# Optimization experiments

Hardware: AMD Instinct MI355X
Metric: run time of the kernel (lower is better)

## Reference

```python
import jax, jax.numpy as jnp
import numpy as np


def setup_inputs() -> dict:
    bs, L, d, h = 4, 1024, 768, 12
    ne, nm, K, P, F, R = 42, 8, 97, 128, 256, 256
    key = jax.random.key(0)
    ks = jax.random.split(key, 16)
    seq = jax.random.normal(ks[0], (bs, L, d), jnp.float32)
    att = jax.random.uniform(ks[1], (bs, h, L, L), jnp.float32)
    mention_pos = jax.random.randint(ks[2], (bs, ne, nm), 0, 1000)
    n_men = jax.random.randint(ks[3], (bs, ne), 1, nm + 1)
    men_mask = (jnp.arange(nm)[None, None, :] < n_men[..., None]).astype(jnp.float32)
    ht_pairs = jax.random.randint(ks[4], (bs, P, 2), 0, ne)
    s = 0.02
    Wattn = jax.random.normal(ks[5], (d, R)) * s
    battn = jnp.zeros((R,), jnp.float32)
    attn_net = jax.random.normal(ks[6], (K, R)) * s
    Wlin = jax.random.normal(ks[7], (d, 3)) * s
    blin = jnp.zeros((3,), jnp.float32)
    Wseg = jax.random.normal(ks[8], (3, 3, 3, F)) * s  # HWIO conv kernel (SegNet stand-in)
    bseg = jnp.zeros((F,), jnp.float32)
    Whead = jax.random.normal(ks[9], (d + F, d)) * s
    bhead = jnp.zeros((d,), jnp.float32)
    Wtail = jax.random.normal(ks[10], (d + F, d)) * s
    btail = jnp.zeros((d,), jnp.float32)
    lim = (1.0 / (2 * d)) ** 0.5
    bilinear = jax.random.uniform(ks[11], (K, d, d), minval=-lim, maxval=lim)
    bilinear_bias = jax.random.uniform(ks[12], (K,), minval=-lim, maxval=lim)
    return dict(sequence_output=seq, attention=att, men_mask=men_mask,
                mention_pos=mention_pos, ht_pairs=ht_pairs,
                Wattn=Wattn, battn=battn, attn_net=attn_net, Wlin=Wlin, blin=blin,
                Wseg=Wseg, bseg=bseg, Whead=Whead, bhead=bhead, Wtail=Wtail,
                btail=btail, bilinear=bilinear, bilinear_bias=bilinear_bias)


def _forward(sequence_output, attention, men_mask, mention_pos, ht_pairs,
             Wattn, battn, attn_net, Wlin, blin, Wseg, bseg,
             Whead, bhead, Wtail, btail, bilinear, bilinear_bias):
    bs, L, d = sequence_output.shape
    h = attention.shape[1]
    ne, nm = mention_pos.shape[1], mention_pos.shape[2]
    K = attn_net.shape[0]
    OFFSET = 1  # BERT [CLS] offset
    pos = jnp.clip(mention_pos + OFFSET, 0, L - 1)           # [bs,ne,nm]
    b_idx = jnp.arange(bs)[:, None, None]
    # ragged mention gather from sequence_output, zero-padded like the torch loops
    emb = sequence_output[b_idx, pos] * men_mask[..., None]  # [bs,ne,nm,d]
    # per-mention attention rows; attention -> [bs,L,h,L] so we gather on token dim
    A = jnp.transpose(attention, (0, 2, 1, 3))
    m_att = A[b_idx, pos] * men_mask[..., None, None]        # [bs,ne,nm,h,L]
    cnt = jnp.maximum(men_mask.sum(-1), 1.0)                 # mentions per entity
    entity_as = m_att.sum(2) / cnt[..., None, None]          # [bs,ne,h,L] mean over mentions
    # label-wise masked attention pooling over mentions
    neg = (1.0 - men_mask)[..., None] * -1e6                 # [bs,ne,nm,1]
    scores = jnp.tanh(emb @ Wattn + battn) @ attn_net.T + neg  # [bs,ne,nm,K]
    w = jax.nn.softmax(scores, axis=-2)                      # softmax over mentions
    entity_es = jnp.einsum('benk,bend->bekd', w, emb)        # [bs,ne,K,d]
    # context-based channel map (pairwise attention overlap, mean over heads)
    ht = jnp.einsum('bihl,bjhl->bijl', entity_as, entity_as) / h  # [bs,ne,ne,L]
    ht = ht / (ht.sum(-1, keepdims=True) + 1e-5)
    fmap = jnp.einsum('bijl,bld->bijd', ht, sequence_output)      # [bs,ne,ne,d]
    x = fmap @ Wlin + blin                                        # [bs,ne,ne,3]
    seg = jax.lax.conv_general_dilated(x, Wseg, (1, 1), 'SAME',
                                       dimension_numbers=('NHWC', 'HWIO', 'NHWC'))
    attn_map = jax.nn.relu(seg + bseg)                            # [bs,ne,ne,F]
    # pairwise gather (get_hts)
    hi, ti = ht_pairs[..., 0], ht_pairs[..., 1]
    bI = jnp.arange(bs)[:, None]
    F = attn_map.shape[-1]
    htss = attn_map[bI, hi, ti].reshape(-1, F)               # [N,F]
    hss = entity_es[bI, hi].reshape(-1, K, d)                # [N,K,d]
    tss = entity_es[bI, ti].reshape(-1, K, d)
    N = hss.shape[0]
    htr = jnp.broadcast_to(htss[:, None, :], (N, K, F))
    hs = jnp.tanh(jnp.concatenate([hss, htr], -1) @ Whead + bhead)
    ts = jnp.tanh(jnp.concatenate([tss, htr], -1) @ Wtail + btail)
    logits = jnp.einsum('nkd,kdp,nkp->nk', hs, bilinear, ts) + bilinear_bias
    return logits


def reference(sequence_output, attention, men_mask, mention_pos, ht_pairs,
              Wattn, battn, attn_net, Wlin, blin, Wseg, bseg,
              Whead, bhead, Wtail, btail, bilinear, bilinear_bias):
    return _forward(sequence_output, attention, men_mask, mention_pos, ht_pairs,
                    Wattn, battn, attn_net, Wlin, blin, Wseg, bseg,
                    Whead, bhead, Wtail, btail, bilinear, bilinear_bias)
```

## Files before the change

### kernel.cpp

```cpp
#include <hip/hip_runtime.h>
#include <hip/hip_bf16.h>

#define BS 4
#define LL 1024
#define DD 768
#define HH 12
#define NE 42
#define NM 8
#define KK 97
#define PPAIR 128
#define FF 256
#define RR 256
#define NPAIR (BS*PPAIR)
#define MROWS (BS*NE*KK)
#define MT 510
#define NT32 16
#define GRID_BG (8*13*16)

typedef __attribute__((ext_vector_type(8))) short short8;
typedef __attribute__((ext_vector_type(16))) float float16;

__device__ __forceinline__ float fast_tanh(float x){
  x = fminf(fmaxf(x, -15.f), 15.f);
  float e = __expf(2.f*x);
  return 1.f - 2.f/(e + 1.f);
}
__device__ __forceinline__ unsigned short f2bf(float f){
  unsigned int u = __float_as_uint(f);
  unsigned int r = (u + 0x7FFF + ((u>>16)&1)) >> 16;
  return (unsigned short)r;
}
__device__ __forceinline__ float bf2f(unsigned short u){
  return __uint_as_float(((unsigned int)u)<<16);
}

__global__ void k_emb(const float* __restrict__ seq, const int* __restrict__ mpos,
                      const float* __restrict__ mask, float* __restrict__ emb){
  int idx = blockIdx.x;
  int t = threadIdx.x;
  int b = idx / (NE*NM);
  float mk = mask[idx];
  int pos = mpos[idx] + 1;
  pos = min(max(pos, 0), LL-1);
  const float* src = seq + ((size_t)b*LL + pos)*DD;
  float* dst = emb + (size_t)idx*DD;
  for (int dd = t; dd < DD; dd += 256) dst[dd] = mk * src[dd];
}

__global__ void k_entity_as(const float* __restrict__ att, const int* __restrict__ mpos,
                            const float* __restrict__ mask, float* __restrict__ eas){
  int idx = blockIdx.x;
  int hh = idx % HH; int be = idx / HH;
  int b = be / NE;
  int t = threadIdx.x;
  float cnt = 0.f;
  for (int m=0;m<NM;m++) cnt += mask[be*NM+m];
  float inv = 1.f / fmaxf(cnt, 1.f);
  float acc[4] = {0.f,0.f,0.f,0.f};
  for (int m=0;m<NM;m++){
    float mk = mask[be*NM+m];
    if (mk != 0.f){
      int pos = min(max(mpos[be*NM+m]+1,0), LL-1);
      const float* row = att + (((size_t)b*HH + hh)*LL + pos)*LL;
      acc[0] += mk*row[t]; acc[1] += mk*row[t+256];
      acc[2] += mk*row[t+512]; acc[3] += mk*row[t+768];
    }
  }
  float* dst = eas + (size_t)idx*LL;
  dst[t]=acc[0]*inv; dst[t+256]=acc[1]*inv; dst[t+512]=acc[2]*inv; dst[t+768]=acc[3]*inv;
}

__global__ void k_score1(const float* __restrict__ emb, const float* __restrict__ Wattn,
                         const float* __restrict__ battn, float* __restrict__ tbuf){
  int idx = blockIdx.x; int t = threadIdx.x;
  __shared__ float es[DD];
  es[t]       = emb[(size_t)idx*DD + t];
  es[t+256]   = emb[(size_t)idx*DD + t + 256];
  es[t+512]   = emb[(size_t)idx*DD + t + 512];
  __syncthreads();
  float acc = battn[t];
  for (int dd=0; dd<DD; dd++) acc += es[dd]*Wattn[dd*RR + t];
  tbuf[(size_t)idx*RR + t] = fast_tanh(acc);
}

__global__ void k_scores(const float* __restrict__ tbuf, const float* __restrict__ an,
                         const float* __restrict__ mask, float* __restrict__ w){
  int be = blockIdx.x; int t = threadIdx.x;
  __shared__ float ts_[NM*RR];
  __shared__ float an_s[64*98];
  for (int i=t; i<NM*RR; i+=128) ts_[i] = tbuf[(size_t)be*NM*RR + i];
  float acc[NM];
  #pragma unroll
  for (int m=0;m<NM;m++) acc[m] = 0.f;
  for (int rc=0; rc<RR; rc+=64){
    __syncthreads();
    for (int i=t; i<KK*64; i+=128){
      int kq = i >> 6, r = i & 63;
      an_s[r*98 + kq] = an[kq*RR + rc + r];
    }
    __syncthreads();
    if (t < KK){
      for (int m=0;m<NM;m++){
        float a = 0.f;
        for (int r=0;r<64;r++) a += ts_[m*RR + rc + r]*an_s[r*98 + t];
        acc[m] += a;
      }
    }
  }
  if (t < KK){
    float s[NM];
    #pragma unroll
    for (int m=0;m<NM;m++){
      float mk = mask[be*NM+m];
      s[m] = acc[m] + (1.f - mk)*(-1e6f);
    }
    float mx = s[0];
    #pragma unroll
    for (int m=1;m<NM;m++) mx = fmaxf(mx, s[m]);
    float sum = 0.f; float e[NM];
    #pragma unroll
    for (int m=0;m<NM;m++){ e[m] = __expf(s[m]-mx); sum += e[m]; }
    float invs = 1.f/sum;
    #pragma unroll
    for (int m=0;m<NM;m++) w[((size_t)be*NM+m)*KK + t] = e[m]*invs;
  }
}

__global__ void k_entity_es(const float* __restrict__ emb, const float* __restrict__ w,
                            unsigned short* __restrict__ esf){
  int be = blockIdx.x; int t = threadIdx.x;
  __shared__ float es[NM*DD];
  __shared__ float ws_[NM*KK];
  for (int i = t; i < NM*DD; i += 256) es[i] = emb[(size_t)be*NM*DD + i];
  for (int i = t; i < NM*KK; i += 256) ws_[i] = w[(size_t)be*NM*KK + i];
  __syncthreads();
  for (int idx = t; idx < KK*96; idx += 256){
    int k = idx % KK, d8 = idx / KK;
    int d0 = d8*8;
    float a[8] = {0,0,0,0,0,0,0,0};
    #pragma unroll
    for (int m=0;m<NM;m++){
      float wv = ws_[m*KK + k];
      #pragma unroll
      for (int j=0;j<8;j++) a[j] += wv*es[m*DD + d0 + j];
    }
    int row = be*KK + k;
    int mt = row >> 5, lr = row & 31, ds = d8 >> 1, qq = d8 & 1;
    short8 v;
    #pragma unroll
    for (int j=0;j<8;j++) v[j] = (short)f2bf(a[j]);
    *(short8*)(esf + ((((size_t)mt*48) + ds)*64 + lr + 32*qq)*8) = v;
  }
}

__global__ void k_seqlin(const float* __restrict__ seq, const float* __restrict__ Wlin,
                         float* __restrict__ sl){
  int bl = blockIdx.x; int t = threadIdx.x;
  const float* row = seq + (size_t)bl*DD;
  float a[3] = {0.f,0.f,0.f};
  for (int dd=t; dd<DD; dd+=256){
    float v = row[dd];
    a[0] += v*Wlin[dd*3+0]; a[1] += v*Wlin[dd*3+1]; a[2] += v*Wlin[dd*3+2];
  }
  __shared__ float red[256];
  float res[3];
  for (int c=0;c<3;c++){
    red[t] = a[c]; __syncthreads();
    for (int off=128; off>0; off>>=1){ if (t<off) red[t]+=red[t+off]; __syncthreads(); }
    res[c] = red[0]; __syncthreads();
  }
  if (t==0){ sl[bl*3+0]=res[0]; sl[bl*3+1]=res[1]; sl[bl*3+2]=res[2]; }
}

__global__ void k_ht_x(const float* __restrict__ eas, const float* __restrict__ sl,
                       const float* __restrict__ blin, float* __restrict__ x){
  int idx = blockIdx.x;
  int j = idx % NE; int i = (idx/NE)%NE; int b = idx/(NE*NE);
  int t = threadIdx.x;
  int w = t >> 6, lane = t & 63;
  const float* ai = eas + ((size_t)(b*NE+i))*HH*LL;
  const float* aj = eas + ((size_t)(b*NE+j))*HH*LL;
  float v[4];
  #pragma unroll
  for (int it=0; it<4; it++){
    int l = t + it*256;
    float acc=0.f;
    #pragma unroll
    for (int hh2=0; hh2<HH; hh2++) acc += ai[hh2*LL + l]*aj[hh2*LL + l];
    v[it] = acc * (1.f/HH);
  }
  __shared__ float wsum[4];
  __shared__ float xred[4][3];
  float s = v[0]+v[1]+v[2]+v[3];
  s += __shfl_xor(s, 1);  s += __shfl_xor(s, 2);  s += __shfl_xor(s, 4);
  s += __shfl_xor(s, 8);  s += __shfl_xor(s, 16); s += __shfl_xor(s, 32);
  if (lane == 0) wsum[w] = s;
  __syncthreads();
  float inv = 1.f/((wsum[0]+wsum[1]+wsum[2]+wsum[3]) + 1e-5f);
  float xa[3]={0.f,0.f,0.f};
  #pragma unroll
  for (int it=0; it<4; it++){
    int l = t + it*256;
    float wv = v[it]*inv;
    const float* s3 = sl + ((size_t)b*LL + l)*3;
    xa[0]+=wv*s3[0]; xa[1]+=wv*s3[1]; xa[2]+=wv*s3[2];
  }
  #pragma unroll
  for (int c=0;c<3;c++){
    float q = xa[c];
    q += __shfl_xor(q, 1);  q += __shfl_xor(q, 2);  q += __shfl_xor(q, 4);
    q += __shfl_xor(q, 8);  q += __shfl_xor(q, 16); q += __shfl_xor(q, 32);
    if (lane == 0) xred[w][c] = q;
  }
  __syncthreads();
  if (t < 3) x[(size_t)idx*3 + t] = xred[0][t]+xred[1][t]+xred[2][t]+xred[3][t] + blin[t];
}

__global__ void k_conv_pairs(const float* __restrict__ x, const int* __restrict__ pairs,
                             const float* __restrict__ Wseg, const float* __restrict__ bseg,
                             float* __restrict__ htss){
  int n = blockIdx.x; int t = threadIdx.x;
  int b = n / PPAIR;
  int hi = pairs[n*2+0], ti = pairs[n*2+1];
  __shared__ float xs[27];
  if (t < 27){
    int di = t/9, dj = (t/3)%3, ci = t%3;
    int ii = hi + di - 1, jj = ti + dj - 1;
    float v = 0.f;
    if (ii>=0 && ii<NE && jj>=0 && jj<NE) v = x[(((size_t)b*NE+ii)*NE+jj)*3 + ci];
    xs[t] = v;
  }
  __syncthreads();
  float acc = bseg[t];
  #pragma unroll
  for (int tap=0; tap<27; tap++) acc += xs[tap]*Wseg[tap*FF + t];
  htss[(size_t)n*FF + t] = fmaxf(acc, 0.f);
}

__global__ void k_pair_proj(const float* __restrict__ htss, const float* __restrict__ Wb,
                            const float* __restrict__ bias, float* __restrict__ outp){
  int n = blockIdx.x; int t = threadIdx.x;
  __shared__ float hs_s[FF];
  hs_s[t] = htss[(size_t)n*FF + t];
  __syncthreads();
  float a0 = bias[t], a1 = bias[t+256], a2 = bias[t+512];
  for (int r=0;r<FF;r++){
    float hv = hs_s[r];
    const float* wr = Wb + (size_t)r*DD;
    a0 += hv*wr[t]; a1 += hv*wr[t+256]; a2 += hv*wr[t+512];
  }
  float* dst = outp + (size_t)n*DD;
  dst[t]=a0; dst[t+256]=a1; dst[t+512]=a2;
}

__global__ void k_wshuffle(const float* __restrict__ src, unsigned short* __restrict__ dst){
  int bi = blockIdx.x;
  int mat = bi / 144; int r = bi % 144;
  int ds = r / 3, ntg = r % 3;
  int t = threadIdx.x;
  size_t mo = (size_t)mat*589824;
  __shared__ float ls[16][260];
  #pragma unroll
  for (int i=0;i<16;i++)
    ls[i][t] = src[mo + ((size_t)(ds*16+i))*768 + ntg*256 + t];
  __syncthreads();
  #pragma unroll
  for (int it=0; it<2; it++){
    int idx = it*256 + t;
    int pt_l = idx >> 6, lane = idx & 63;
    int nl = pt_l*32 + (lane & 31);
    int qq = lane >> 5;
    short8 v;
    #pragma unroll
    for (int j=0;j<8;j++) v[j] = (short)f2bf(ls[qq*8 + j][nl]);
    *(short8*)(dst + mo + (((size_t)ds*24 + ntg*8 + pt_l)*64 + lane)*8) = v;
  }
}

__global__ __launch_bounds__(256) void k_gemm_frag(const unsigned short* __restrict__ Af,
    const unsigned short* __restrict__ Bf, unsigned short* __restrict__ C){
  int mt = blockIdx.x / 6, ntg = blockIdx.x % 6;
  int t = threadIdx.x; int w = t >> 6; int lane = t & 63;
  int nt = ntg*4 + w;
  float16 acc = (float16)(0.0f);
  const unsigned short* ap = Af + (((size_t)mt*48)*64 + lane)*8;
  const unsigned short* bp = Bf + (((size_t)nt)*64 + lane)*8;
  #pragma unroll 4
  for (int ds=0; ds<48; ds++){
    short8 a = *(const short8*)(ap + (size_t)ds*512);
    short8 b = *(const short8*)(bp + (size_t)ds*24*512);
    acc = __builtin_amdgcn_mfma_f32_32x32x16_bf16(a, b, acc, 0, 0, 0);
  }
  int col = nt*32 + (lane & 31);
  int aq = lane >> 5;
  #pragma unroll
  for (int rI=0;rI<16;rI++){
    int row = mt*32 + (rI&3) + 8*(rI>>2) + 4*aq;
    C[(size_t)row*768 + col] = f2bf(acc[rI]);
  }
}

__global__ void k_hsts(const unsigned short* __restrict__ Ehb, const float* __restrict__ ph,
                       const int* __restrict__ pairs, unsigned short* __restrict__ hsF){
  int bi = blockIdx.x; int nt = bi / KK; int k = bi - nt*KK;
  int t = threadIdx.x;
  __shared__ int ehB[32];
  if (t < 32){
    int n = nt*32 + t; int b = n >> 7;
    ehB[t] = ((b*NE + pairs[n*2+0])*KK + k)*DD;
  }
  __syncthreads();
  unsigned short* dst = hsF + (((size_t)nt*KK + k)*48)*512;
  #pragma unroll 2
  for (int c=0; c<12; c++){
    int L = c*256 + t;
    int ds = L >> 6, lane = L & 63;
    int r = lane & 31, q = lane >> 5;
    int n = nt*32 + r;
    int d0 = ds*16 + q*8;
    short8 ev = *(const short8*)(Ehb + ehB[r] + d0);
    float4 p0 = *(const float4*)(ph + (size_t)n*DD + d0);
    float4 p1 = *(const float4*)(ph + (size_t)n*DD + d0 + 4);
    float pf[8] = {p0.x,p0.y,p0.z,p0.w,p1.x,p1.y,p1.z,p1.w};
    short8 v;
    #pragma unroll
    for (int j=0;j<8;j++) v[j] = (short)f2bf(fast_tanh(bf2f((unsigned short)ev[j]) + pf[j]));
    *(short8*)(dst + (size_t)ds*512 + lane*8) = v;
  }
}

__global__ void k_outinit(const float* __restrict__ bias, float* __restrict__ out){
  int i = blockIdx.x*256 + threadIdx.x;
  if (i < NPAIR*KK) out[i] = bias[i % KK];
}

__global__ __launch_bounds__(512,4) void k_bil_gemm(
    const unsigned short* __restrict__ hsF, const unsigned short* __restrict__ Etb,
    const float* __restrict__ pt_, const unsigned short* __restrict__ Bfrag,
    const int* __restrict__ pairs, float* __restrict__ out){
  int xcd = blockIdx.x & 7; int g = blockIdx.x >> 3;
  int ps = g & 3; int nt = (g >> 2) & 3; int kgrp = g >> 4;
  int k = kgrp*8 + xcd;
  if (k >= KK) return;
  int n0 = nt*128;
  int t = threadIdx.x; int w = t >> 6; int lane = t & 63;
  int wr = w >> 1, wc = w & 1;
  __shared__ int etB[128];
  __shared__ float redbuf[4][2][32];
  if (t < 128){
    int n = n0 + t; int b = n >> 7;
    etB[t] = ((b*NE + pairs[n*2+1])*KK + k)*DD;
  }
  __syncthreads();
  int aq = lane >> 5;
  int mt = nt*4 + wr;
  const unsigned short* ap = hsF + (((size_t)mt*KK + k)*48)*512 + lane*8;
  const unsigned short* bb = Bfrag + (size_t)k*589824 + (size_t)lane*8;
  int pb0 = ps*6 + wc;
  float16 acc0 = (float16)(0.f), acc1 = (float16)(0.f), acc2 = (float16)(0.f);
  #pragma unroll 4
  for (int ds=0; ds<48; ds++){
    short8 a = *(const short8*)(ap + (size_t)ds*512);
    const unsigned short* bds = bb + (size_t)ds*24*512;
    short8 b0 = *(const short8*)(bds + (size_t)(pb0+0)*512);
    short8 b1 = *(const short8*)(bds + (size_t)(pb0+2)*512);
    short8 b2 = *(const short8*)(bds + (size_t)(pb0+4)*512);
    acc0 = __builtin_amdgcn_mfma_f32_32x32x16_bf16(a, b0, acc0, 0, 0, 0);
    acc1 = __builtin_amdgcn_mfma_f32_32x32x16_bf16(a, b1, acc1, 0, 0, 0);
    acc2 = __builtin_amdgcn_mfma_f32_32x32x16_bf16(a, b2, acc2, 0, 0, 0);
  }
  #pragma unroll
  for (int rI=0; rI<16; rI++){
    int row = (rI&3) + 8*(rI>>2) + 4*aq;
    int nloc = wr*32 + row;
    int eb = etB[nloc];
    const float* ptp = pt_ + (size_t)(n0 + nloc)*DD;
    int colb = lane & 31;
    int c0 = (pb0+0)*32 + colb, c1 = (pb0+2)*32 + colb, c2 = (pb0+4)*32 + colb;
    float s = acc0[rI]*fast_tanh(bf2f(Etb[eb + c0]) + ptp[c0])
            + acc1[rI]*fast_tanh(bf2f(Etb[eb + c1]) + ptp[c1])
            + acc2[rI]*fast_tanh(bf2f(Etb[eb + c2]) + ptp[c2]);
    s += __shfl_xor(s, 1);  s += __shfl_xor(s, 2);
    s += __shfl_xor(s, 4);  s += __shfl_xor(s, 8);
    s += __shfl_xor(s, 16);
    if ((lane & 31) == 0) redbuf[wr][wc][row] = s;
  }
  __syncthreads();
  if (t < 128){
    atomicAdd(&out[(size_t)(n0 + t)*KK + k],
              redbuf[t>>5][0][t&31] + redbuf[t>>5][1][t&31]);
  }
}

extern "C" void kernel_launch(void* const* d_in, const int* in_sizes, int n_in,
                              void* d_out, int out_size, void* d_ws, size_t ws_size,
                              hipStream_t stream){
  const float* seq      = (const float*)d_in[0];
  const float* att      = (const float*)d_in[1];
  const float* mask     = (const float*)d_in[2];
  const int*   mpos     = (const int*)d_in[3];
  const int*   pairs    = (const int*)d_in[4];
  const float* Wattn    = (const float*)d_in[5];
  const float* battn    = (const float*)d_in[6];
  const float* attn_net = (const float*)d_in[7];
  const float* Wlin     = (const float*)d_in[8];
  const float* blin     = (const float*)d_in[9];
  const float* Wseg     = (const float*)d_in[10];
  const float* bseg     = (const float*)d_in[11];
  const float* Whead    = (const float*)d_in[12];
  const float* bhead    = (const float*)d_in[13];
  const float* Wtail    = (const float*)d_in[14];
  const float* btail    = (const float*)d_in[15];
  const float* bil      = (const float*)d_in[16];
  const float* bilb     = (const float*)d_in[17];
  float* out = (float*)d_out;

  char* ws = (char*)d_ws;
  size_t off = 0;
  auto allocB = [&](size_t nbytes)->char*{
    char* p = ws + off;
    off += (nbytes + 255) & ~(size_t)255;
    return p;
  };
  unsigned short* BF     = (unsigned short*)allocB((size_t)KK*589824*2);
  unsigned short* Ehb    = (unsigned short*)allocB((size_t)MT*32*768*2);
  unsigned short* Etb    = (unsigned short*)allocB((size_t)MT*32*768*2);
  unsigned short* WheadF = (unsigned short*)allocB((size_t)589824*2);
  unsigned short* WtailF = (unsigned short*)allocB((size_t)589824*2);
  float* phb  = (float*)allocB((size_t)NPAIR*DD*4);
  float* ptb  = (float*)allocB((size_t)NPAIR*DD*4);
  size_t hsF_bytes = (size_t)NT32*KK*48*512*2;
  char* uni = allocB(hsF_bytes);
  size_t uoff = 0;
  auto ualloc = [&](size_t nbytes)->char*{
    char* p = uni + uoff;
    uoff += (nbytes + 255) & ~(size_t)255;
    return p;
  };
  float* emb  = (float*)ualloc((size_t)BS*NE*NM*DD*4);
  float* tbuf = (float*)ualloc((size_t)BS*NE*NM*RR*4);
  float* wsm  = (float*)ualloc((size_t)BS*NE*NM*KK*4);
  float* eas  = (float*)ualloc((size_t)BS*NE*HH*LL*4);
  float* sl   = (float*)ualloc((size_t)BS*LL*3*4);
  float* xb   = (float*)ualloc((size_t)BS*NE*NE*3*4);
  float* htss = (float*)ualloc((size_t)NPAIR*FF*4);
  unsigned short* esf = (unsigned short*)ualloc((size_t)MT*48*64*8*2);
  unsigned short* hsF = (unsigned short*)uni;

  k_outinit<<<(NPAIR*KK+255)/256, 256, 0, stream>>>(bilb, out);
  k_emb<<<BS*NE*NM, 256, 0, stream>>>(seq, mpos, mask, emb);
  k_score1<<<BS*NE*NM, 256, 0, stream>>>(emb, Wattn, battn, tbuf);
  k_scores<<<BS*NE, 128, 0, stream>>>(tbuf, attn_net, mask, wsm);
  k_entity_as<<<BS*NE*HH, 256, 0, stream>>>(att, mpos, mask, eas);
  k_entity_es<<<BS*NE, 256, 0, stream>>>(emb, wsm, esf);
  k_seqlin<<<BS*LL, 256, 0, stream>>>(seq, Wlin, sl);
  k_ht_x<<<BS*NE*NE, 256, 0, stream>>>(eas, sl, blin, xb);
  k_conv_pairs<<<NPAIR, 256, 0, stream>>>(xb, pairs, Wseg, bseg, htss);
  k_pair_proj<<<NPAIR, 256, 0, stream>>>(htss, Whead + 768*768, bhead, phb);
  k_pair_proj<<<NPAIR, 256, 0, stream>>>(htss, Wtail + 768*768, btail, ptb);
  k_wshuffle<<<144, 256, 0, stream>>>(Whead, WheadF);
  k_wshuffle<<<144, 256, 0, stream>>>(Wtail, WtailF);
  k_wshuffle<<<KK*144, 256, 0, stream>>>(bil, BF);
  k_gemm_frag<<<MT*6, 256, 0, stream>>>(esf, WheadF, Ehb);
  k_gemm_frag<<<MT*6, 256, 0, stream>>>(esf, WtailF, Etb);
  k_hsts<<<NT32*KK, 256, 0, stream>>>(Ehb, phb, pairs, hsF);
  k_bil_gemm<<<GRID_BG, 512, 0, stream>>>(hsF, Etb, ptb, BF, pairs, out);
}
```

Before: 970.6 us.

## Stage bilinear GEMM tiles via LDS double buffering and fuse head/tail GEMMs

In the bilinear GEMM, operand fragments were loaded redundantly from global memory by each wave. They are now loaded once per block into LDS using async global_load_lds, with a two-stage double buffer and barriers. The head and tail projection GEMMs also merge into one kernel that reuses the A fragment for both weight sets. The aim is to cut global memory traffic and launches, at the cost of two barriers per k-step and hand-written waitcnt bookkeeping.

New measurement: 892.9 us. 1.09x faster.

```diff
diff --git a/kernel.cpp b/kernel.cpp
--- a/kernel.cpp
+++ b/kernel.cpp
@@ -32,6 +32,11 @@
 }
 __device__ __forceinline__ float bf2f(unsigned short u){
   return __uint_as_float(((unsigned int)u)<<16);
+}
+__device__ __forceinline__ void stage16(const void* g, void* l){
+  __builtin_amdgcn_global_load_lds(
+      (const __attribute__((address_space(1))) void*)g,
+      (__attribute__((address_space(3))) void*)l, 16, 0, 0);
 }
 
 __global__ void k_emb(const float* __restrict__ seq, const int* __restrict__ mpos,
@@ -277,26 +282,31 @@
   }
 }
 
-__global__ __launch_bounds__(256) void k_gemm_frag(const unsigned short* __restrict__ Af,
-    const unsigned short* __restrict__ Bf, unsigned short* __restrict__ C){
+__global__ __launch_bounds__(256) void k_gemm_frag2(const unsigned short* __restrict__ Af,
+    const unsigned short* __restrict__ Bh, const unsigned short* __restrict__ Bt,
+    unsigned short* __restrict__ Ch, unsigned short* __restrict__ Ct){
   int mt = blockIdx.x / 6, ntg = blockIdx.x % 6;
   int t = threadIdx.x; int w = t >> 6; int lane = t & 63;
   int nt = ntg*4 + w;
-  float16 acc = (float16)(0.0f);
+  float16 acch = (float16)(0.0f), acct = (float16)(0.0f);
   const unsigned short* ap = Af + (((size_t)mt*48)*64 + lane)*8;
-  const unsigned short* bp = Bf + (((size_t)nt)*64 + lane)*8;
+  const unsigned short* bph = Bh + (((size_t)nt)*64 + lane)*8;
+  const unsigned short* bpt = Bt + (((size_t)nt)*64 + lane)*8;
   #pragma unroll 4
   for (int ds=0; ds<48; ds++){
-    short8 a = *(const short8*)(ap + (size_t)ds*512);
-    short8 b = *(const short8*)(bp + (size_t)ds*24*512);
-    acc = __builtin_amdgcn_mfma_f32_32x32x16_bf16(a, b, acc, 0, 0, 0);
+    short8 a  = *(const short8*)(ap + (size_t)ds*512);
+    short8 bh = *(const short8*)(bph + (size_t)ds*24*512);
+    short8 bt = *(const short8*)(bpt + (size_t)ds*24*512);
+    acch = __builtin_amdgcn_mfma_f32_32x32x16_bf16(a, bh, acch, 0, 0, 0);
+    acct = __builtin_amdgcn_mfma_f32_32x32x16_bf16(a, bt, acct, 0, 0, 0);
   }
   int col = nt*32 + (lane & 31);
   int aq = lane >> 5;
   #pragma unroll
   for (int rI=0;rI<16;rI++){
     int row = mt*32 + (rI&3) + 8*(rI>>2) + 4*aq;
-    C[(size_t)row*768 + col] = f2bf(acc[rI]);
+    Ch[(size_t)row*768 + col] = f2bf(acch[rI]);
+    Ct[(size_t)row*768 + col] = f2bf(acct[rI]);
   }
 }
 
@@ -346,6 +356,8 @@
   int t = threadIdx.x; int w = t >> 6; int lane = t & 63;
   int wr = w >> 1, wc = w & 1;
   __shared__ int etB[128];
+  __shared__ unsigned short aS[2][4][512];
+  __shared__ unsigned short bS[2][6][512];
   __shared__ float redbuf[4][2][32];
   if (t < 128){
     int n = n0 + t; int b = n >> 7;
@@ -353,22 +365,51 @@
   }
   __syncthreads();
   int aq = lane >> 5;
-  int mt = nt*4 + wr;
-  const unsigned short* ap = hsF + (((size_t)mt*KK + k)*48)*512 + lane*8;
-  const unsigned short* bb = Bfrag + (size_t)k*589824 + (size_t)lane*8;
-  int pb0 = ps*6 + wc;
+  const unsigned short* gp0;
+  unsigned short* lp0s[2];
+  const unsigned short* gp1 = nullptr;
+  unsigned short* lp1s[2] = {nullptr, nullptr};
+  size_t gstep0, gstep1 = 0;
+  if (w < 4){
+    gp0 = hsF + (((size_t)(nt*4 + w)*KK + k)*48)*512 + lane*8;
+    gstep0 = 512;
+    lp0s[0] = &aS[0][w][0]; lp0s[1] = &aS[1][w][0];
+  } else {
+    gp0 = Bfrag + ((size_t)k*1152 + (size_t)(ps*6 + (w-4)))*512 + lane*8;
+    gstep0 = 24*512;
+    lp0s[0] = &bS[0][w-4][0]; lp0s[1] = &bS[1][w-4][0];
+  }
+  int nch = 1;
+  if (w < 2){
+    gp1 = Bfrag + ((size_t)k*1152 + (size_t)(ps*6 + 4 + w))*512 + lane*8;
+    gstep1 = 24*512;
+    lp1s[0] = &bS[0][4+w][0]; lp1s[1] = &bS[1][4+w][0];
+    nch = 2;
+  }
   float16 acc0 = (float16)(0.f), acc1 = (float16)(0.f), acc2 = (float16)(0.f);
-  #pragma unroll 4
+  stage16(gp0, lp0s[0]);
+  if (nch == 2) stage16(gp1, lp1s[0]);
   for (int ds=0; ds<48; ds++){
-    short8 a = *(const short8*)(ap + (size_t)ds*512);
-    const unsigned short* bds = bb + (size_t)ds*24*512;
-    short8 b0 = *(const short8*)(bds + (size_t)(pb0+0)*512);
-    short8 b1 = *(const short8*)(bds + (size_t)(pb0+2)*512);
-    short8 b2 = *(const short8*)(bds + (size_t)(pb0+4)*512);
+    int buf = ds & 1;
+    if (ds < 47){
+      stage16(gp0 + (size_t)(ds+1)*gstep0, lp0s[buf^1]);
+      if (nch == 2) stage16(gp1 + (size_t)(ds+1)*gstep1, lp1s[buf^1]);
+      if (nch == 2) asm volatile("s_waitcnt vmcnt(2)" ::: "memory");
+      else          asm volatile("s_waitcnt vmcnt(1)" ::: "memory");
+    } else {
+      asm volatile("s_waitcnt vmcnt(0)" ::: "memory");
+    }
+    asm volatile("s_barrier" ::: "memory");
+    short8 a  = *(const short8*)&aS[buf][wr][lane*8];
+    short8 b0 = *(const short8*)&bS[buf][wc  ][lane*8];
+    short8 b1 = *(const short8*)&bS[buf][wc+2][lane*8];
+    short8 b2 = *(const short8*)&bS[buf][wc+4][lane*8];
     acc0 = __builtin_amdgcn_mfma_f32_32x32x16_bf16(a, b0, acc0, 0, 0, 0);
     acc1 = __builtin_amdgcn_mfma_f32_32x32x16_bf16(a, b1, acc1, 0, 0, 0);
     acc2 = __builtin_amdgcn_mfma_f32_32x32x16_bf16(a, b2, acc2, 0, 0, 0);
-  }
+    asm volatile("s_barrier" ::: "memory");
+  }
+  int pb0 = ps*6 + wc;
   #pragma unroll
   for (int rI=0; rI<16; rI++){
     int row = (rI&3) + 8*(rI>>2) + 4*aq;
@@ -461,8 +502,7 @@
   k_wshuffle<<<144, 256, 0, stream>>>(Whead, WheadF);
   k_wshuffle<<<144, 256, 0, stream>>>(Wtail, WtailF);
   k_wshuffle<<<KK*144, 256, 0, stream>>>(bil, BF);
-  k_gemm_frag<<<MT*6, 256, 0, stream>>>(esf, WheadF, Ehb);
-  k_gemm_frag<<<MT*6, 256, 0, stream>>>(esf, WtailF, Etb);
+  k_gemm_frag2<<<MT*6, 256, 0, stream>>>(esf, WheadF, WtailF, Ehb, Etb);
   k_hsts<<<NT32*KK, 256, 0, stream>>>(Ehb, phb, pairs, hsF);
   k_bil_gemm<<<GRID_BG, 512, 0, stream>>>(hsF, Etb, ptb, BF, pairs, out);
 }
```
